# Kernel tuning notes

Hardware: AMD Instinct MI355X
Metric: run time of the kernel (lower is better)

Reference implementation:

```python
import jax, jax.numpy as jnp
import numpy as np

MIN_BIN_W = 1e-3
MIN_BIN_H = 1e-3
MIN_DERIV = 1e-3
EPS = 1e-6


def _mlp(x, W0, b0, W1, b1, W2, b2):
    h = jax.nn.relu(x @ W0 + b0)
    h = jax.nn.relu(h @ W1 + b1)
    return h @ W2 + b2


def _rqs_forward(inputs, widths, heights, derivatives):
    # inputs: [B, D]; widths/heights: [B, D, nb]; derivatives: [B, D, nb-1]
    nb = widths.shape[-1]
    inputs = jnp.clip(inputs, 0.0, 1.0)
    widths = jax.nn.softmax(widths, axis=-1)
    heights = jax.nn.softmax(heights, axis=-1)
    widths = MIN_BIN_W + (1.0 - MIN_BIN_W * nb) * widths
    heights = MIN_BIN_H + (1.0 - MIN_BIN_H * nb) * heights
    derivatives = jax.nn.softplus(derivatives) + MIN_DERIV

    pad2 = [(0, 0), (0, 0)]
    x_knots = jnp.pad(jnp.cumsum(widths, axis=-1), pad2 + [(1, 0)])   # [B,D,nb+1]
    y_knots = jnp.pad(jnp.cumsum(heights, axis=-1), pad2 + [(1, 0)])
    derivs = jnp.pad(derivatives, pad2 + [(1, 1)], constant_values=1.0)  # [B,D,nb+1]

    # searchsorted (side='left'): count of knots strictly less than input
    bin_idx = jnp.sum(x_knots < inputs[..., None], axis=-1)
    bin_idx = jnp.clip(bin_idx, 1, nb)[..., None]  # [B,D,1]

    g = lambda a, i: jnp.take_along_axis(a, i, axis=-1)[..., 0]
    x_k = g(x_knots, bin_idx - 1)
    y_k = g(y_knots, bin_idx - 1)
    w_k = g(widths, bin_idx - 1)
    h_k = g(heights, bin_idx - 1)
    d_k = g(derivs, bin_idx - 1)
    d_k1 = g(derivs, bin_idx)

    s_k = h_k / w_k
    theta = (inputs - x_k) / w_k
    t1t = theta * (1.0 - theta)
    den = s_k + (d_k + d_k1 - 2.0 * s_k) * t1t
    outputs = y_k + h_k * (s_k * theta ** 2 + d_k * t1t) / (den + EPS)
    nom_d = s_k ** 2 * (d_k1 * theta ** 2 + 2.0 * s_k * t1t + d_k * (1.0 - theta) ** 2)
    log_det = jnp.log(nom_d / (den ** 2 + EPS))
    return outputs, log_det


def setup_inputs() -> dict:
    key = jax.random.key(0)
    ks = jax.random.split(key, 7)
    B, D, H, NB = 65536, 64, 512, 8
    out_dim = D * (3 * NB - 1)
    inp = {
        "x": jax.random.uniform(ks[0], (B, D), dtype=jnp.float32),
        "W0": jax.random.normal(ks[1], (D, H), dtype=jnp.float32) * 0.05,
        "b0": jnp.zeros((H,), jnp.float32),
        "W1": jax.random.normal(ks[2], (H, H), dtype=jnp.float32) * 0.05,
        "b1": jnp.zeros((H,), jnp.float32),
        "W2": jax.random.normal(ks[3], (H, out_dim), dtype=jnp.float32) * 0.05,
        "b2": jnp.zeros((out_dim,), jnp.float32),
        "num_bins": NB,
    }
    return inp


def reference(x, W0, b0, W1, b1, W2, b2, num_bins):
    B, D = x.shape
    nb = int(num_bins)
    params = _mlp(x, W0, b0, W1, b1, W2, b2).reshape(B, D, 3 * nb - 1)
    widths = params[..., :nb]
    heights = params[..., nb:2 * nb]
    derivatives = params[..., 2 * nb:]
    z, log_det = _rqs_forward(x, widths, heights, derivatives)
    return z, jnp.sum(log_det, axis=1)
```

## Files before the change

kernel.cpp:

```cpp
#include <hip/hip_runtime.h>

typedef unsigned short u16;
typedef __bf16 bf16x8 __attribute__((ext_vector_type(8)));
typedef float f32x4 __attribute__((ext_vector_type(4)));

__device__ __forceinline__ u16 f2bf_r(float f) {
    union { float f; unsigned u; } v; v.f = f;
    return (u16)((v.u + 0x8000u) >> 16);
}
__device__ __forceinline__ float rcpf(float x) { return __builtin_amdgcn_rcpf(x); }

__device__ __forceinline__ void gload_lds16(const u16* g, u16* l) {
    __builtin_amdgcn_global_load_lds(
        (const __attribute__((address_space(1))) void*)g,
        (__attribute__((address_space(3))) void*)l,
        16, 0, 0);
}


#define BM 128
#define BN 128
#define BK 32

template<int K, int RELU, int NBX>
__global__ __launch_bounds__(256) void gemm_bt(
    const u16* __restrict__ A, const u16* __restrict__ BT,
    const float* __restrict__ bias, u16* __restrict__ C,
    int M, int N)
{
    constexpr int NS = K / BK;
    __shared__ u16 smem[3 * 8192];
    const int t = threadIdx.x;
    const int lane = t & 63;
    const int wave = t >> 6;
    const int wr = (wave >> 1) * 64;
    const int wc = (wave & 1) * 64;

    const int nlin = blockIdx.x;
    const int jj = nlin >> 3;
    const long brow = (long)((nlin & 7) + 8 * (jj / NBX)) * BM;
    const long bcol = (long)(jj % NBX) * BN;

    const int sr = t >> 2;
    const int sc = ((t & 3) ^ ((t >> 3) & 3)) * 8;
    const u16* gA0 = A + (brow + sr) * (long)K + sc;
    const u16* gA1 = gA0 + 64L * K;
    const u16* gB0 = BT + (bcol + sr) * (long)K + sc;
    const u16* gB1 = gB0 + 64L * K;

    f32x4 acc[4][4] = {};
    const int fr = lane & 15;
    const int fbase = fr * 32 + (((lane >> 4) ^ ((fr >> 1) & 3)) * 8);

    auto STAGE = [&](int buf, int k0) {
        u16* As = &smem[buf * 8192];
        u16* Bs = As + 4096;
        gload_lds16(gA0 + k0, &As[t * 8]);
        gload_lds16(gA1 + k0, &As[2048 + t * 8]);
        gload_lds16(gB0 + k0, &Bs[t * 8]);
        gload_lds16(gB1 + k0, &Bs[2048 + t * 8]);
    };
    auto COMPUTE = [&](int buf) {
        const u16* As = &smem[buf * 8192];
        const u16* Bs = As + 4096;
        bf16x8 af[4], bfr[4];
#pragma unroll
        for (int m = 0; m < 4; ++m)
            af[m] = *(const bf16x8*)&As[wr * 32 + m * 512 + fbase];
#pragma unroll
        for (int n = 0; n < 4; ++n)
            bfr[n] = *(const bf16x8*)&Bs[wc * 32 + n * 512 + fbase];
#pragma unroll
        for (int m = 0; m < 4; ++m)
#pragma unroll
            for (int n = 0; n < 4; ++n)
                acc[m][n] = __builtin_amdgcn_mfma_f32_16x16x32_bf16(
                    af[m], bfr[n], acc[m][n], 0, 0, 0);
    };

    STAGE(0, 0);
    STAGE(1, BK);
#pragma unroll
    for (int i = 0; i < NS; ++i) {
        if (i < NS - 1) asm volatile("s_waitcnt vmcnt(4)" ::: "memory");
        else            asm volatile("s_waitcnt vmcnt(0)" ::: "memory");
        __builtin_amdgcn_s_barrier();
        __builtin_amdgcn_sched_barrier(0);
        if (i + 2 < NS) STAGE((i + 2) % 3, (i + 2) * BK);
        COMPUTE(i % 3);
    }

#pragma unroll
    for (int n = 0; n < 4; ++n) {
        const long col = bcol + wc + n * 16 + fr;
        const float bv = bias[col];
#pragma unroll
        for (int m = 0; m < 4; ++m) {
            const long row = brow + wr + m * 16 + (lane >> 4) * 4;
#pragma unroll
            for (int j = 0; j < 4; ++j) {
                float v = acc[m][n][j] + bv;
                if (RELU) v = fmaxf(v, 0.f);
                C[(row + j) * (long)N + col] = f2bf_r(v);
            }
        }
    }
}

#define FBM 128
#define FBN 192
#define FBK 32
#define CLS 200

template<int K>
__global__ __launch_bounds__(256) void gemm3_rqs(
    const u16* __restrict__ A,
    const u16* __restrict__ BT,
    const float* __restrict__ bias,
    const float* __restrict__ x,
    float* __restrict__ z,
    float* __restrict__ ldp)
{
    constexpr int NS = K / FBK;
    __shared__ u16 smem[3 * 10240];
    const int t = threadIdx.x;
    const int lane = t & 63;
    const int wave = t >> 6;
    const int wr = (wave >> 1) * 64;
    const int wc = (wave & 1) * 96;

    const int nlin = blockIdx.x;
    const int jj = nlin >> 3;
    const long brow = (long)((nlin & 7) + 8 * (jj >> 3)) * FBM;
    const int bx = jj & 7;
    const int bcol = bx * FBN;

    const int sr = t >> 2;
    const int sc = ((t & 3) ^ ((t >> 3) & 3)) * 8;
    const u16* gA0 = A + (brow + sr) * (long)K + sc;
    const u16* gB0 = BT + (long)(bcol + sr) * K + sc;

    f32x4 acc[4][6] = {};
    const int fr = lane & 15;
    const int gsel = ((lane >> 4) ^ ((fr >> 1) & 3)) * 8;
    const int fbase = fr * 32 + gsel;

    int b_off[6];
#pragma unroll
    for (int n = 0; n < 6; ++n) {
        int rb = wc + n * 16 + fr;
        b_off[n] = (rb >> 6) * 2048 + (rb & 63) * 32 + gsel;
    }

    auto STAGE = [&](int buf, int k0) {
        u16* As = &smem[buf * 10240];
        u16* Bs = As + 4096;
        gload_lds16(gA0 + k0,            &As[t * 8]);
        gload_lds16(gA0 + 64L * K + k0,  &As[2048 + t * 8]);
        gload_lds16(gB0 + k0,            &Bs[t * 8]);
        gload_lds16(gB0 + 64L * K + k0,  &Bs[2048 + t * 8]);
        gload_lds16(gB0 + 128L * K + k0, &Bs[4096 + t * 8]);
    };
    auto COMPUTE = [&](int buf) {
        const u16* As = &smem[buf * 10240];
        const u16* Bs = As + 4096;
        bf16x8 af[4], bfr[6];
#pragma unroll
        for (int m = 0; m < 4; ++m)
            af[m] = *(const bf16x8*)&As[wr * 32 + m * 512 + fbase];
#pragma unroll
        for (int n = 0; n < 6; ++n)
            bfr[n] = *(const bf16x8*)&Bs[b_off[n]];
#pragma unroll
        for (int m = 0; m < 4; ++m)
#pragma unroll
            for (int n = 0; n < 6; ++n)
                acc[m][n] = __builtin_amdgcn_mfma_f32_16x16x32_bf16(
                    af[m], bfr[n], acc[m][n], 0, 0, 0);
    };

    STAGE(0, 0);
    STAGE(1, FBK);
#pragma unroll
    for (int i = 0; i < NS; ++i) {
        if (i < NS - 1) asm volatile("s_waitcnt vmcnt(5)" ::: "memory");
        else            asm volatile("s_waitcnt vmcnt(0)" ::: "memory");
        __builtin_amdgcn_s_barrier();
        __builtin_amdgcn_sched_barrier(0);
        if (i + 2 < NS) STAGE((i + 2) % 3, (i + 2) * FBK);
        COMPUTE(i % 3);
    }
    __syncthreads();

#pragma unroll
    for (int n = 0; n < 6; ++n) {
        const int cl = wc + n * 16 + fr;
        const float bv = bias[bcol + cl];
#pragma unroll
        for (int m = 0; m < 4; ++m) {
            const int rl = wr + m * 16 + (lane >> 4) * 4;
#pragma unroll
            for (int j = 0; j < 4; ++j)
                smem[(rl + j) * CLS + cl] = f2bf_r(acc[m][n][j] + bv);
        }
    }
    __syncthreads();

    const int dbase = bx * 8;
#pragma unroll
    for (int pi = 0; pi < 4; ++pi) {
        const int p  = t + pi * 256;
        const int bl = p >> 3;
        const int dl = p & 7;
        const u16* pp = &smem[bl * CLS + dl * 24];
        bf16x8 v0 = *(const bf16x8*)(pp);
        bf16x8 v1 = *(const bf16x8*)(pp + 8);
        bf16x8 v2 = *(const bf16x8*)(pp + 16);

        float w[8], h[8];
        float sw = 0.f, sh = 0.f;
#pragma unroll
        for (int i = 0; i < 8; ++i) { w[i] = __expf((float)v0[i]); sw += w[i]; }
#pragma unroll
        for (int i = 0; i < 8; ++i) { h[i] = __expf((float)v1[i]); sh += h[i]; }
        const float rw = 0.992f * rcpf(sw);
        const float rh = 0.992f * rcpf(sh);
#pragma unroll
        for (int i = 0; i < 8; ++i) w[i] = fmaf(w[i], rw, 0.001f);
#pragma unroll
        for (int i = 0; i < 8; ++i) h[i] = fmaf(h[i], rh, 0.001f);

        const long b = brow + bl;
        const int  d = dbase + dl;
        float xin = x[b * 64 + d];
        xin = fminf(fmaxf(xin, 0.f), 1.f);

        float x_k = 0.f, y_k = 0.f, w_k = w[0], h_k = h[0];
        float rk = 0.f, rk1 = (float)v2[0];
        bool isfirst = true, islast = false;
        float cw = 0.f, ch = 0.f;
#pragma unroll
        for (int i = 1; i < 8; ++i) {
            cw += w[i - 1]; ch += h[i - 1];
            if (cw < xin) {
                x_k = cw; y_k = ch; w_k = w[i]; h_k = h[i];
                rk = (float)v2[i - 1];
                rk1 = (i < 7) ? (float)v2[i] : 0.f;
                isfirst = false; islast = (i == 7);
            }
        }
        float sp_k  = __logf(1.f + __expf(rk));
        float sp_k1 = __logf(1.f + __expf(rk1));
        float d_k  = isfirst ? 1.f : sp_k  + 0.001f;
        float d_k1 = islast  ? 1.f : sp_k1 + 0.001f;

        const float inv_wk = rcpf(w_k);
        const float s   = h_k * inv_wk;
        const float th  = (xin - x_k) * inv_wk;
        const float omt = 1.f - th;
        const float t1t = th * omt;
        const float den = fmaf(d_k + d_k1 - 2.f * s, t1t, s);
        const float num = fmaf(s * th, th, d_k * t1t);
        const float out = fmaf(h_k * num, rcpf(den + 1e-6f), y_k);
        const float nom = s * s * fmaf(d_k1 * th, th, fmaf(2.f * s, t1t, d_k * omt * omt));
        const float logdet = __logf(nom) - __logf(fmaf(den, den, 1e-6f));

        z[b * 64 + d]   = out;
        ldp[b * 64 + d] = logdet;
    }
}

__global__ __launch_bounds__(256) void ld_reduce(
    const float* __restrict__ ldp, float* __restrict__ ld)
{
    const int b = blockIdx.x * 4 + (threadIdx.x >> 6);
    const int lane = threadIdx.x & 63;
    float r = ldp[(long)b * 64 + lane];
#pragma unroll
    for (int off = 32; off; off >>= 1) r += __shfl_xor(r, off, 64);
    if (lane == 0) ld[b] = r;
}

__global__ void cvt_x_bf16(const float* __restrict__ in, u16* __restrict__ out, long n) {
    long i = (long)blockIdx.x * blockDim.x + threadIdx.x;
    long stride = (long)gridDim.x * blockDim.x;
    for (; i < n; i += stride) out[i] = f2bf_r(in[i]);
}

__global__ void transpose_w_bf16(const float* __restrict__ W, u16* __restrict__ WT,
                                 int K, int N) {
    long total = (long)N * K;
    long i = (long)blockIdx.x * blockDim.x + threadIdx.x;
    long stride = (long)gridDim.x * blockDim.x;
    for (; i < total; i += stride) {
        int n = (int)(i / K), k = (int)(i % K);
        WT[i] = f2bf_r(W[(long)k * N + n]);
    }
}

__global__ void transpose_w2_bf16(const float* __restrict__ W, u16* __restrict__ WT, int K) {
    long total = 1536L * K;
    long i = (long)blockIdx.x * blockDim.x + threadIdx.x;
    long stride = (long)gridDim.x * blockDim.x;
    for (; i < total; i += stride) {
        int npad = (int)(i / K), k = (int)(i % K);
        int g = npad / 24, r = npad % 24;
        float v = (r < 23) ? W[(long)k * 1472 + g * 23 + r] : 0.f;
        WT[i] = f2bf_r(v);
    }
}

__global__ void pad_bias2(const float* __restrict__ b2, float* __restrict__ b2p) {
    int c = blockIdx.x * 256 + threadIdx.x;
    if (c < 1536) {
        int g = c / 24, r = c % 24;
        b2p[c] = (r < 23) ? b2[g * 23 + r] : 0.f;
    }
}

__global__ void fill_fail(float* __restrict__ out, long n) {
    long i = (long)blockIdx.x * blockDim.x + threadIdx.x;
    long stride = (long)gridDim.x * blockDim.x;
    for (; i < n; i += stride) out[i] = -1.0f;
}

extern "C" void kernel_launch(void* const* d_in, const int* in_sizes, int n_in,
                              void* d_out, int out_size, void* d_ws, size_t ws_size,
                              hipStream_t stream)
{
    const float* x  = (const float*)d_in[0];
    const float* W0 = (const float*)d_in[1];
    const float* b0 = (const float*)d_in[2];
    const float* W1 = (const float*)d_in[3];
    const float* b1 = (const float*)d_in[4];
    const float* W2 = (const float*)d_in[5];
    const float* b2 = (const float*)d_in[6];
    const int B = in_sizes[0] / 64;
    const int D = 64, H = 512, NP = 1536;

    char* ws = (char*)d_ws;
    size_t off = 0;
    u16* W0T = (u16*)(ws + off); off += (size_t)H * D * 2;
    u16* W1T = (u16*)(ws + off); off += (size_t)H * H * 2;
    u16* W2T = (u16*)(ws + off); off += (size_t)NP * H * 2;
    float* b2p = (float*)(ws + off); off += (size_t)NP * 4;
    off = (off + 255) & ~(size_t)255;
    u16*   h1  = (u16*)(ws + off);
    float* ldp = (float*)(ws + off);
    off += (size_t)B * H * 2;
    u16* xb = (u16*)(ws + off);
    u16* h2 = (u16*)(ws + off);
    off += (size_t)B * H * 2;
    size_t need = off;

    float* zout  = (float*)d_out;
    float* ldout = zout + (size_t)B * D;

    if (ws_size < need) {
        fill_fail<<<2048, 256, 0, stream>>>(zout, (long)out_size);
        return;
    }

    cvt_x_bf16<<<2048, 256, 0, stream>>>(x, xb, (long)B * D);
    transpose_w_bf16<<<128, 256, 0, stream>>>(W0, W0T, D, H);
    transpose_w_bf16<<<1024, 256, 0, stream>>>(W1, W1T, H, H);
    transpose_w2_bf16<<<3072, 256, 0, stream>>>(W2, W2T, H);
    pad_bias2<<<6, 256, 0, stream>>>(b2, b2p);

    gemm_bt<64, 1, 4><<<2048, 256, 0, stream>>>(xb, W0T, b0, h1, B, H);
    gemm_bt<512, 1, 4><<<2048, 256, 0, stream>>>(h1, W1T, b1, h2, B, H);

    gemm3_rqs<512><<<4096, 256, 0, stream>>>(h2, W2T, b2p, x, zout, ldp);

    ld_reduce<<<B / 4, 256, 0, stream>>>(ldp, ldout);
}
```

Baseline: 210.2 us.

## Enlarge fused GEMM3+RQS tile to 256x192x64 with 8 waves and interleaved LDS/MFMA schedule

The fused final GEMM and spline kernel moves from 128x192 tiles with 4 waves and a triple buffer to 256x192x64 tiles with 8 waves and a double buffer. Inside each K step, LDS fragment reads for the next quarter are interleaved with MFMA blocks, with s_setprio raised around the MFMAs, to overlap LDS latency with matrix math. Larger tiles cut redundant B reads per row and halve the block count. In exchange the kernel uses more LDS and registers per block, which may limit occupancy, and the epilogue now reuses a larger shared buffer.

```diff
diff --git a/kernel.cpp b/kernel.cpp
--- a/kernel.cpp
+++ b/kernel.cpp
@@ -107,13 +107,15 @@
     }
 }
 
-#define FBM 128
-#define FBN 192
-#define FBK 32
+#define G3_BM 256
+#define G3_BN 192
+#define G3_BK 64
+#define G3_BUF 28672
+#define G3_BOFF 16384
 #define CLS 200
 
 template<int K>
-__global__ __launch_bounds__(256) void gemm3_rqs(
+__global__ __launch_bounds__(512, 2) void gemm3_rqs(
     const u16* __restrict__ A,
     const u16* __restrict__ BT,
     const float* __restrict__ bias,
@@ -121,87 +123,126 @@
     float* __restrict__ z,
     float* __restrict__ ldp)
 {
-    constexpr int NS = K / FBK;
-    __shared__ u16 smem[3 * 10240];
+    constexpr int NT = K / G3_BK;
+    __shared__ u16 smem[2 * G3_BUF];
+
     const int t = threadIdx.x;
     const int lane = t & 63;
     const int wave = t >> 6;
-    const int wr = (wave >> 1) * 64;
-    const int wc = (wave & 1) * 96;
+    const int wm = wave >> 2;
+    const int wn = wave & 3;
 
     const int nlin = blockIdx.x;
-    const int jj = nlin >> 3;
-    const long brow = (long)((nlin & 7) + 8 * (jj >> 3)) * FBM;
-    const int bx = jj & 7;
-    const int bcol = bx * FBN;
-
-    const int sr = t >> 2;
-    const int sc = ((t & 3) ^ ((t >> 3) & 3)) * 8;
-    const u16* gA0 = A + (brow + sr) * (long)K + sc;
-    const u16* gB0 = BT + (long)(bcol + sr) * K + sc;
-
-    f32x4 acc[4][6] = {};
+    const int bx = (nlin >> 3) & 7;
+    const long BROW = ((long)(nlin & 7) + 8 * (nlin >> 6)) * G3_BM;
+    const int bcol = bx * G3_BN;
+
+    const int rowp = (t & 255) >> 2;
+    const int kcol = (((t & 3) ^ ((t >> 3) & 3)) * 8) + ((t & 256) ? 32 : 0);
+    const u16* gA = A + (BROW + rowp) * (long)K + kcol;
+    const u16* gB = BT + ((long)bcol + rowp) * K + kcol;
+
+    f32x4 acc[8][3] = {};
     const int fr = lane & 15;
     const int gsel = ((lane >> 4) ^ ((fr >> 1) & 3)) * 8;
-    const int fbase = fr * 32 + gsel;
-
-    int b_off[6];
-#pragma unroll
-    for (int n = 0; n < 6; ++n) {
-        int rb = wc + n * 16 + fr;
-        b_off[n] = (rb >> 6) * 2048 + (rb & 63) * 32 + gsel;
-    }
-
-    auto STAGE = [&](int buf, int k0) {
-        u16* As = &smem[buf * 10240];
-        u16* Bs = As + 4096;
-        gload_lds16(gA0 + k0,            &As[t * 8]);
-        gload_lds16(gA0 + 64L * K + k0,  &As[2048 + t * 8]);
-        gload_lds16(gB0 + k0,            &Bs[t * 8]);
-        gload_lds16(gB0 + 64L * K + k0,  &Bs[2048 + t * 8]);
-        gload_lds16(gB0 + 128L * K + k0, &Bs[4096 + t * 8]);
+
+    int a_off[8];
+#pragma unroll
+    for (int m = 0; m < 8; ++m) {
+        int ra = wm * 128 + m * 16 + fr;
+        a_off[m] = (ra >> 6) * 4096 + (ra & 63) * 32 + gsel;
+    }
+    int b_off[3];
+#pragma unroll
+    for (int nn = 0; nn < 3; ++nn) {
+        int rb = wn * 48 + nn * 16 + fr;
+        b_off[nn] = G3_BOFF + (rb >> 6) * 4096 + (rb & 63) * 32 + gsel;
+    }
+
+    auto STAGE = [&](int tile, int buf) {
+        const long ko = (long)tile * G3_BK;
+        u16* dst = &smem[buf * G3_BUF];
+#pragma unroll
+        for (int r = 0; r < 4; ++r)
+            gload_lds16(gA + ko + (long)r * 64 * K, &dst[r * 4096 + t * 8]);
+#pragma unroll
+        for (int r = 0; r < 3; ++r)
+            gload_lds16(gB + ko + (long)r * 64 * K, &dst[G3_BOFF + r * 4096 + t * 8]);
     };
-    auto COMPUTE = [&](int buf) {
-        const u16* As = &smem[buf * 10240];
-        const u16* Bs = As + 4096;
-        bf16x8 af[4], bfr[6];
-#pragma unroll
-        for (int m = 0; m < 4; ++m)
-            af[m] = *(const bf16x8*)&As[wr * 32 + m * 512 + fbase];
-#pragma unroll
-        for (int n = 0; n < 6; ++n)
-            bfr[n] = *(const bf16x8*)&Bs[b_off[n]];
-#pragma unroll
-        for (int m = 0; m < 4; ++m)
-#pragma unroll
-            for (int n = 0; n < 6; ++n)
-                acc[m][n] = __builtin_amdgcn_mfma_f32_16x16x32_bf16(
-                    af[m], bfr[n], acc[m][n], 0, 0, 0);
+
+    bf16x8 bfr[3][2], afA[2][2], afB[2][2];
+    auto READ_A = [&](bf16x8 (&af)[2][2], int q, const u16* Ab) {
+#pragma unroll
+        for (int md = 0; md < 2; ++md)
+#pragma unroll
+            for (int h = 0; h < 2; ++h)
+                af[md][h] = *(const bf16x8*)&Ab[a_off[q * 2 + md] + h * 2048];
     };
+    auto MFMA_Q = [&](bf16x8 (&af)[2][2], int q) {
+#pragma unroll
+        for (int md = 0; md < 2; ++md)
+#pragma unroll
+            for (int nn = 0; nn < 3; ++nn)
+#pragma unroll
+                for (int h = 0; h < 2; ++h)
+                    acc[q * 2 + md][nn] = __builtin_amdgcn_mfma_f32_16x16x32_bf16(
+                        af[md][h], bfr[nn][h], acc[q * 2 + md][nn], 0, 0, 0);
+    };
 
     STAGE(0, 0);
-    STAGE(1, FBK);
-#pragma unroll
-    for (int i = 0; i < NS; ++i) {
-        if (i < NS - 1) asm volatile("s_waitcnt vmcnt(5)" ::: "memory");
+    STAGE(1, 1);
+    asm volatile("s_waitcnt vmcnt(7)" ::: "memory");
+    __builtin_amdgcn_s_barrier();
+    __builtin_amdgcn_sched_barrier(0);
+
+#pragma unroll
+    for (int i = 0; i < NT; ++i) {
+        const int cur = i & 1;
+        const u16* Ab = &smem[cur * G3_BUF];
+
+#pragma unroll
+        for (int nn = 0; nn < 3; ++nn)
+#pragma unroll
+            for (int h = 0; h < 2; ++h)
+                bfr[nn][h] = *(const bf16x8*)&Ab[b_off[nn] + h * 2048];
+        READ_A(afA, 0, Ab);
+        READ_A(afB, 1, Ab);
+        __builtin_amdgcn_s_setprio(1); MFMA_Q(afA, 0); __builtin_amdgcn_s_setprio(0);
+        __builtin_amdgcn_s_barrier();
+        __builtin_amdgcn_sched_barrier(0);
+
+        READ_A(afA, 2, Ab);
+        __builtin_amdgcn_s_setprio(1); MFMA_Q(afB, 1); __builtin_amdgcn_s_setprio(0);
+        __builtin_amdgcn_s_barrier();
+        __builtin_amdgcn_sched_barrier(0);
+
+        READ_A(afB, 3, Ab);
+        __builtin_amdgcn_s_setprio(1); MFMA_Q(afA, 2); __builtin_amdgcn_s_setprio(0);
+        asm volatile("s_waitcnt lgkmcnt(0)" ::: "memory");
+        __builtin_amdgcn_sched_barrier(0);
+        __builtin_amdgcn_s_barrier();
+        __builtin_amdgcn_sched_barrier(0);
+
+        if (i + 2 < NT) STAGE(i + 2, cur);
+        __builtin_amdgcn_s_setprio(1); MFMA_Q(afB, 3); __builtin_amdgcn_s_setprio(0);
+        if (i < NT - 2) asm volatile("s_waitcnt vmcnt(7)" ::: "memory");
         else            asm volatile("s_waitcnt vmcnt(0)" ::: "memory");
         __builtin_amdgcn_s_barrier();
         __builtin_amdgcn_sched_barrier(0);
-        if (i + 2 < NS) STAGE((i + 2) % 3, (i + 2) * FBK);
-        COMPUTE(i % 3);
-    }
+    }
+
     __syncthreads();
 
 #pragma unroll
-    for (int n = 0; n < 6; ++n) {
-        const int cl = wc + n * 16 + fr;
+    for (int nn = 0; nn < 3; ++nn) {
+        const int cl = wn * 48 + nn * 16 + fr;
         const float bv = bias[bcol + cl];
 #pragma unroll
-        for (int m = 0; m < 4; ++m) {
-            const int rl = wr + m * 16 + (lane >> 4) * 4;
+        for (int m = 0; m < 8; ++m) {
+            const int rl = wm * 128 + m * 16 + (lane >> 4) * 4;
 #pragma unroll
             for (int j = 0; j < 4; ++j)
-                smem[(rl + j) * CLS + cl] = f2bf_r(acc[m][n][j] + bv);
+                smem[(rl + j) * CLS + cl] = f2bf_r(acc[m][nn][j] + bv);
         }
     }
     __syncthreads();
@@ -209,7 +250,7 @@
     const int dbase = bx * 8;
 #pragma unroll
     for (int pi = 0; pi < 4; ++pi) {
-        const int p  = t + pi * 256;
+        const int p  = t + pi * 512;
         const int bl = p >> 3;
         const int dl = p & 7;
         const u16* pp = &smem[bl * CLS + dl * 24];
@@ -230,7 +271,7 @@
 #pragma unroll
         for (int i = 0; i < 8; ++i) h[i] = fmaf(h[i], rh, 0.001f);
 
-        const long b = brow + bl;
+        const long b = BROW + bl;
         const int  d = dbase + dl;
         float xin = x[b * 64 + d];
         xin = fminf(fmaxf(xin, 0.f), 1.f);
@@ -370,7 +411,7 @@
     gemm_bt<64, 1, 4><<<2048, 256, 0, stream>>>(xb, W0T, b0, h1, B, H);
     gemm_bt<512, 1, 4><<<2048, 256, 0, stream>>>(h1, W1T, b1, h2, B, H);
 
-    gemm3_rqs<512><<<4096, 256, 0, stream>>>(h2, W2T, b2p, x, zout, ldp);
+    gemm3_rqs<512><<<2048, 512, 0, stream>>>(h2, W2T, b2p, x, zout, ldp);
 
     ld_reduce<<<B / 4, 256, 0, stream>>>(ldp, ldout);
 }
```

Result: slower. 232.8 us (+10.7%).

## Enlarge fused GEMM3 tile to 256 rows with 512 threads; merge prep kernels

Applied to the files above, without the earlier changes.

The final GEMM+RQS kernel now uses 256x192 tiles with 8 waves, so each staged B tile is shared by twice as many rows. This halves the grid and cuts redundant weight loads. Loading is split across the two 256-thread halves, with per-half vmcnt waits, and the LDS buffer is enlarged to hold the staging epilogue. Separately, the five weight and input conversion kernels are merged into one launch with a vectorised x conversion to cut launch overhead. The trade-off is higher LDS use (about 100KB) and register pressure with launch_bounds(512,2), which could limit occupancy.

```diff
diff --git a/kernel.cpp b/kernel.cpp
--- a/kernel.cpp
+++ b/kernel.cpp
@@ -107,13 +107,15 @@
     }
 }
 
-#define FBM 128
-#define FBN 192
-#define FBK 32
+#define G3_BM 256
+#define G3_BN 192
+#define G3_BK 32
+#define G3_BUF 14336
+#define G3_BOFF 8192
 #define CLS 200
 
 template<int K>
-__global__ __launch_bounds__(256) void gemm3_rqs(
+__global__ __launch_bounds__(512, 2) void gemm3_rqs(
     const u16* __restrict__ A,
     const u16* __restrict__ BT,
     const float* __restrict__ bias,
@@ -121,8 +123,9 @@
     float* __restrict__ z,
     float* __restrict__ ldp)
 {
-    constexpr int NS = K / FBK;
-    __shared__ u16 smem[3 * 10240];
+    constexpr int NS = K / G3_BK;
+    __shared__ u16 smem[G3_BM * CLS];
+
     const int t = threadIdx.x;
     const int lane = t & 63;
     const int wave = t >> 6;
@@ -130,78 +133,89 @@
     const int wc = (wave & 1) * 96;
 
     const int nlin = blockIdx.x;
-    const int jj = nlin >> 3;
-    const long brow = (long)((nlin & 7) + 8 * (jj >> 3)) * FBM;
-    const int bx = jj & 7;
-    const int bcol = bx * FBN;
-
-    const int sr = t >> 2;
-    const int sc = ((t & 3) ^ ((t >> 3) & 3)) * 8;
-    const u16* gA0 = A + (brow + sr) * (long)K + sc;
-    const u16* gB0 = BT + (long)(bcol + sr) * K + sc;
+    const int bx = (nlin >> 3) & 7;
+    const long BROW = ((long)(nlin & 7) + 8 * (nlin >> 6)) * G3_BM;
+    const int bcol = bx * G3_BN;
+
+    const int tt = t & 255;
+    const int thi = t >> 8;
+    const int sr = tt >> 2;
+    const int sc = ((tt & 3) ^ ((tt >> 3) & 3)) * 8;
+    const u16* gA = A + (BROW + sr) * (long)K + sc;
+    const u16* gB = BT + ((long)bcol + sr) * K + sc;
 
     f32x4 acc[4][6] = {};
     const int fr = lane & 15;
     const int gsel = ((lane >> 4) ^ ((fr >> 1) & 3)) * 8;
-    const int fbase = fr * 32 + gsel;
-
+
+    int a_off[4];
+#pragma unroll
+    for (int m = 0; m < 4; ++m) {
+        int ra = wr + m * 16 + fr;
+        a_off[m] = (ra >> 6) * 2048 + (ra & 63) * 32 + gsel;
+    }
     int b_off[6];
 #pragma unroll
-    for (int n = 0; n < 6; ++n) {
-        int rb = wc + n * 16 + fr;
-        b_off[n] = (rb >> 6) * 2048 + (rb & 63) * 32 + gsel;
+    for (int nn = 0; nn < 6; ++nn) {
+        int rb = wc + nn * 16 + fr;
+        b_off[nn] = G3_BOFF + (rb >> 6) * 2048 + (rb & 63) * 32 + gsel;
     }
 
     auto STAGE = [&](int buf, int k0) {
-        u16* As = &smem[buf * 10240];
-        u16* Bs = As + 4096;
-        gload_lds16(gA0 + k0,            &As[t * 8]);
-        gload_lds16(gA0 + 64L * K + k0,  &As[2048 + t * 8]);
-        gload_lds16(gB0 + k0,            &Bs[t * 8]);
-        gload_lds16(gB0 + 64L * K + k0,  &Bs[2048 + t * 8]);
-        gload_lds16(gB0 + 128L * K + k0, &Bs[4096 + t * 8]);
+        u16* dst = &smem[buf * G3_BUF];
+        gload_lds16(gA + (long)(thi) * 64 * K + k0,     &dst[(thi) * 2048 + tt * 8]);
+        gload_lds16(gA + (long)(thi + 2) * 64 * K + k0, &dst[(thi + 2) * 2048 + tt * 8]);
+        if (thi == 0) {
+            gload_lds16(gB + k0,                 &dst[G3_BOFF + tt * 8]);
+            gload_lds16(gB + 128L * K + k0,      &dst[G3_BOFF + 2 * 2048 + tt * 8]);
+        } else {
+            gload_lds16(gB + 64L * K + k0,       &dst[G3_BOFF + 2048 + tt * 8]);
+        }
     };
     auto COMPUTE = [&](int buf) {
-        const u16* As = &smem[buf * 10240];
-        const u16* Bs = As + 4096;
+        const u16* Ab = &smem[buf * G3_BUF];
         bf16x8 af[4], bfr[6];
 #pragma unroll
         for (int m = 0; m < 4; ++m)
-            af[m] = *(const bf16x8*)&As[wr * 32 + m * 512 + fbase];
-#pragma unroll
-        for (int n = 0; n < 6; ++n)
-            bfr[n] = *(const bf16x8*)&Bs[b_off[n]];
+            af[m] = *(const bf16x8*)&Ab[a_off[m]];
+#pragma unroll
+        for (int nn = 0; nn < 6; ++nn)
+            bfr[nn] = *(const bf16x8*)&Ab[b_off[nn]];
 #pragma unroll
         for (int m = 0; m < 4; ++m)
 #pragma unroll
-            for (int n = 0; n < 6; ++n)
-                acc[m][n] = __builtin_amdgcn_mfma_f32_16x16x32_bf16(
-                    af[m], bfr[n], acc[m][n], 0, 0, 0);
+            for (int nn = 0; nn < 6; ++nn)
+                acc[m][nn] = __builtin_amdgcn_mfma_f32_16x16x32_bf16(
+                    af[m], bfr[nn], acc[m][nn], 0, 0, 0);
     };
 
     STAGE(0, 0);
-    STAGE(1, FBK);
+    STAGE(1, G3_BK);
 #pragma unroll
     for (int i = 0; i < NS; ++i) {
-        if (i < NS - 1) asm volatile("s_waitcnt vmcnt(5)" ::: "memory");
-        else            asm volatile("s_waitcnt vmcnt(0)" ::: "memory");
+        if (i < NS - 1) {
+            if (thi == 0) asm volatile("s_waitcnt vmcnt(4)" ::: "memory");
+            else          asm volatile("s_waitcnt vmcnt(3)" ::: "memory");
+        } else {
+            asm volatile("s_waitcnt vmcnt(0)" ::: "memory");
+        }
         __builtin_amdgcn_s_barrier();
         __builtin_amdgcn_sched_barrier(0);
-        if (i + 2 < NS) STAGE((i + 2) % 3, (i + 2) * FBK);
+        if (i + 2 < NS) STAGE((i + 2) % 3, (i + 2) * G3_BK);
         COMPUTE(i % 3);
     }
     __syncthreads();
 
 #pragma unroll
-    for (int n = 0; n < 6; ++n) {
-        const int cl = wc + n * 16 + fr;
+    for (int nn = 0; nn < 6; ++nn) {
+        const int cl = wc + nn * 16 + fr;
         const float bv = bias[bcol + cl];
 #pragma unroll
         for (int m = 0; m < 4; ++m) {
             const int rl = wr + m * 16 + (lane >> 4) * 4;
 #pragma unroll
             for (int j = 0; j < 4; ++j)
-                smem[(rl + j) * CLS + cl] = f2bf_r(acc[m][n][j] + bv);
+                smem[(rl + j) * CLS + cl] = f2bf_r(acc[m][nn][j] + bv);
         }
     }
     __syncthreads();
@@ -209,7 +223,7 @@
     const int dbase = bx * 8;
 #pragma unroll
     for (int pi = 0; pi < 4; ++pi) {
-        const int p  = t + pi * 256;
+        const int p  = t + pi * 512;
         const int bl = p >> 3;
         const int dl = p & 7;
         const u16* pp = &smem[bl * CLS + dl * 24];
@@ -230,7 +244,7 @@
 #pragma unroll
         for (int i = 0; i < 8; ++i) h[i] = fmaf(h[i], rh, 0.001f);
 
-        const long b = brow + bl;
+        const long b = BROW + bl;
         const int  d = dbase + dl;
         float xin = x[b * 64 + d];
         xin = fminf(fmaxf(xin, 0.f), 1.f);
@@ -281,40 +295,45 @@
     if (lane == 0) ld[b] = r;
 }
 
-__global__ void cvt_x_bf16(const float* __restrict__ in, u16* __restrict__ out, long n) {
-    long i = (long)blockIdx.x * blockDim.x + threadIdx.x;
-    long stride = (long)gridDim.x * blockDim.x;
-    for (; i < n; i += stride) out[i] = f2bf_r(in[i]);
-}
-
-__global__ void transpose_w_bf16(const float* __restrict__ W, u16* __restrict__ WT,
-                                 int K, int N) {
-    long total = (long)N * K;
-    long i = (long)blockIdx.x * blockDim.x + threadIdx.x;
-    long stride = (long)gridDim.x * blockDim.x;
-    for (; i < total; i += stride) {
-        int n = (int)(i / K), k = (int)(i % K);
-        WT[i] = f2bf_r(W[(long)k * N + n]);
-    }
-}
-
-__global__ void transpose_w2_bf16(const float* __restrict__ W, u16* __restrict__ WT, int K) {
-    long total = 1536L * K;
-    long i = (long)blockIdx.x * blockDim.x + threadIdx.x;
-    long stride = (long)gridDim.x * blockDim.x;
-    for (; i < total; i += stride) {
-        int npad = (int)(i / K), k = (int)(i % K);
-        int g = npad / 24, r = npad % 24;
-        float v = (r < 23) ? W[(long)k * 1472 + g * 23 + r] : 0.f;
-        WT[i] = f2bf_r(v);
-    }
-}
-
-__global__ void pad_bias2(const float* __restrict__ b2, float* __restrict__ b2p) {
-    int c = blockIdx.x * 256 + threadIdx.x;
-    if (c < 1536) {
-        int g = c / 24, r = c % 24;
-        b2p[c] = (r < 23) ? b2[g * 23 + r] : 0.f;
+__global__ __launch_bounds__(256) void prep_all(
+    const float* __restrict__ x,  u16* __restrict__ xb,
+    const float* __restrict__ W0, u16* __restrict__ W0T,
+    const float* __restrict__ W1, u16* __restrict__ W1T,
+    const float* __restrict__ W2, u16* __restrict__ W2T,
+    const float* __restrict__ b2, float* __restrict__ b2p)
+{
+    const int bid = blockIdx.x;
+    const int t = threadIdx.x;
+    if (bid < 2048) {
+        const long i8 = ((long)bid * 256 + t) * 8;
+        const f32x4 v0 = *(const f32x4*)&x[i8];
+        const f32x4 v1 = *(const f32x4*)&x[i8 + 4];
+        u16 o[8];
+#pragma unroll
+        for (int j = 0; j < 4; ++j) o[j] = f2bf_r(v0[j]);
+#pragma unroll
+        for (int j = 0; j < 4; ++j) o[4 + j] = f2bf_r(v1[j]);
+        *(ulong2*)&xb[i8] = *(const ulong2*)o;
+    } else if (bid < 2176) {
+        const int i = (bid - 2048) * 256 + t;
+        const int n = i >> 6, k = i & 63;
+        W0T[i] = f2bf_r(W0[k * 512 + n]);
+    } else if (bid < 3200) {
+        const int i = (bid - 2176) * 256 + t;
+        const int n = i >> 9, k = i & 511;
+        W1T[i] = f2bf_r(W1[k * 512 + n]);
+    } else if (bid < 6272) {
+        const int i = (bid - 3200) * 256 + t;
+        const int npad = i >> 9, k = i & 511;
+        const int g = npad / 24, r = npad % 24;
+        float v = (r < 23) ? W2[(long)k * 1472 + g * 23 + r] : 0.f;
+        W2T[i] = f2bf_r(v);
+    } else {
+        const int c = (bid - 6272) * 256 + t;
+        if (c < 1536) {
+            const int g = c / 24, r = c % 24;
+            b2p[c] = (r < 23) ? b2[g * 23 + r] : 0.f;
+        }
     }
 }
 
@@ -361,16 +380,12 @@
         return;
     }
 
-    cvt_x_bf16<<<2048, 256, 0, stream>>>(x, xb, (long)B * D);
-    transpose_w_bf16<<<128, 256, 0, stream>>>(W0, W0T, D, H);
-    transpose_w_bf16<<<1024, 256, 0, stream>>>(W1, W1T, H, H);
-    transpose_w2_bf16<<<3072, 256, 0, stream>>>(W2, W2T, H);
-    pad_bias2<<<6, 256, 0, stream>>>(b2, b2p);
+    prep_all<<<6278, 256, 0, stream>>>(x, xb, W0, W0T, W1, W1T, W2, W2T, b2, b2p);
 
     gemm_bt<64, 1, 4><<<2048, 256, 0, stream>>>(xb, W0T, b0, h1, B, H);
     gemm_bt<512, 1, 4><<<2048, 256, 0, stream>>>(h1, W1T, b1, h2, B, H);
 
-    gemm3_rqs<512><<<4096, 256, 0, stream>>>(h2, W2T, b2p, x, zout, ldp);
+    gemm3_rqs<512><<<2048, 512, 0, stream>>>(h2, W2T, b2p, x, zout, ldp);
 
     ld_reduce<<<B / 4, 256, 0, stream>>>(ldp, ldout);
 }
```

After: 213.2 us. Within noise of the previous version (+1.4%).
